# Optimization experiments

Measured on AMD Instinct MI355X. Metric: run time of the kernel, lower is better.

The kernel has to match this reference:

```python
import jax, jax.numpy as jnp
import numpy as np

B, S, HID = 2, 2048, 2560
NH, NKV, HD = 32, 8, 128
GROUPS = NH // NKV  # 4
THETA = 1000000.0
EPS = 1e-6


def setup_inputs() -> dict:
    key = jax.random.key(0)
    ks = jax.random.split(key, 6)
    inp = {
        "hidden_states": jax.random.normal(ks[0], (B, S, HID), jnp.float32),
        "Wq": jax.random.normal(ks[1], (HID, NH * HD), jnp.float32) * 0.02,
        "Wk": jax.random.normal(ks[2], (HID, NKV * HD), jnp.float32) * 0.02,
        "Wv": jax.random.normal(ks[3], (HID, NKV * HD), jnp.float32) * 0.02,
        "Wo": jax.random.normal(ks[4], (NH * HD, HID), jnp.float32) * 0.02,
        "q_norm_w": jnp.ones((HD,), jnp.float32),
        "k_norm_w": jnp.ones((HD,), jnp.float32),
        "position_ids": jnp.broadcast_to(jnp.arange(S, dtype=jnp.int64 if jax.config.jax_enable_x64 else jnp.int32), (B, S)),
    }
    return inp


def _rms_norm(x, w, eps=EPS):
    # per-head-dim RMSNorm in fp32, matching Qwen3RMSNorm
    xf = x.astype(jnp.float32)
    var = jnp.mean(xf * xf, axis=-1, keepdims=True)
    return (w * (xf * jax.lax.rsqrt(var + eps))).astype(x.dtype)


def _rotate_half(x):
    x1, x2 = jnp.split(x, 2, axis=-1)
    return jnp.concatenate((-x2, x1), axis=-1)


def _rope_tables(seq_len, pos_ids):
    inv_freq = 1.0 / (THETA ** (jnp.arange(0, HD, 2, dtype=jnp.float32) / HD))
    t = jnp.arange(seq_len, dtype=jnp.float32)
    freqs = jnp.einsum("i,j->ij", t, inv_freq)           # [S, HD/2]
    emb = jnp.concatenate((freqs, freqs), axis=-1)        # [S, HD]
    cos = jnp.cos(emb)[pos_ids][:, None, :, :]            # [B,1,S,HD]
    sin = jnp.sin(emb)[pos_ids][:, None, :, :]
    return cos, sin


def _attention(hidden_states, Wq, Wk, Wv, Wo, q_norm_w, k_norm_w, position_ids):
    b, s, _ = hidden_states.shape
    q = (hidden_states @ Wq).reshape(b, s, NH, HD).transpose(0, 2, 1, 3)   # [B,NH,S,HD]
    k = (hidden_states @ Wk).reshape(b, s, NKV, HD).transpose(0, 2, 1, 3)  # [B,NKV,S,HD]
    v = (hidden_states @ Wv).reshape(b, s, NKV, HD).transpose(0, 2, 1, 3)
    q = _rms_norm(q, q_norm_w)
    k = _rms_norm(k, k_norm_w)
    cos, sin = _rope_tables(s, position_ids)
    q = q * cos + _rotate_half(q) * sin
    k = k * cos + _rotate_half(k) * sin
    # GQA: group queries instead of repeating K/V (same math as repeat_kv)
    qg = q.reshape(b, NKV, GROUPS, s, HD)
    scale = 1.0 / np.sqrt(HD)
    scores = jnp.einsum("bhgqd,bhkd->bhgqk", qg, k) * scale  # [B,NKV,G,S,S]
    causal = jnp.tril(jnp.ones((s, s), bool))
    scores = jnp.where(causal, scores, jnp.finfo(scores.dtype).min)
    probs = jax.nn.softmax(scores.astype(jnp.float32), axis=-1).astype(q.dtype)
    out = jnp.einsum("bhgqk,bhkd->bhgqd", probs, v)          # [B,NKV,G,S,HD]
    out = out.reshape(b, NH, s, HD).transpose(0, 2, 1, 3).reshape(b, s, NH * HD)
    return out @ Wo                                          # [B,S,HID]


def reference(hidden_states, Wq, Wk, Wv, Wo, q_norm_w, k_norm_w, position_ids):
    return _attention(hidden_states, Wq, Wk, Wv, Wo, q_norm_w, k_norm_w, position_ids)
```

## Files before the change

### kernel.cpp

```cpp
#include <hip/hip_runtime.h>
#include <hip/hip_bf16.h>
#include <math.h>

#define B_ 2
#define S_ 2048
#define HID_ 2560
#define NH_ 32
#define NKV_ 8
#define HD_ 128

typedef __attribute__((ext_vector_type(8))) short bf16x8;
typedef __attribute__((ext_vector_type(4))) float f32x4;

union U8 { bf16x8 v; unsigned short u[8]; };

__device__ __forceinline__ unsigned short f2bf(float x) {
    unsigned u = __float_as_uint(x);
    u = u + 0x7FFF + ((u >> 16) & 1);
    return (unsigned short)(u >> 16);
}
__device__ __forceinline__ float bf2f(unsigned short h) {
    return __uint_as_float(((unsigned)h) << 16);
}

#define GL16(g, l)                                                             \
    __builtin_amdgcn_global_load_lds(                                          \
        (const __attribute__((address_space(1))) void*)(g),                    \
        (__attribute__((address_space(3))) void*)(l), 16, 0, 0)

__global__ void rope_table_kernel(float* __restrict__ cost, float* __restrict__ sint) {
    int t = blockIdx.x;
    int j = threadIdx.x;
    float invf = (float)pow(1.0e6, -(double)j / 64.0);
    float ang  = (float)t * invf;
    cost[t * 64 + j] = cosf(ang);
    sint[t * 64 + j] = sinf(ang);
}

__global__ __launch_bounds__(256) void convert_split(const float* __restrict__ in,
                                                     unsigned short* __restrict__ hi,
                                                     unsigned short* __restrict__ lo,
                                                     int n4) {
    int i = blockIdx.x * 256 + threadIdx.x;
    if (i >= n4) return;
    float4 v = *(const float4*)(in + (size_t)i * 4);
    ushort4 h, l;
    h.x = f2bf(v.x); l.x = f2bf(v.x - bf2f(h.x));
    h.y = f2bf(v.y); l.y = f2bf(v.y - bf2f(h.y));
    h.z = f2bf(v.z); l.z = f2bf(v.z - bf2f(h.z));
    h.w = f2bf(v.w); l.w = f2bf(v.w - bf2f(h.w));
    *(ushort4*)(hi + (size_t)i * 4) = h;
    *(ushort4*)(lo + (size_t)i * 4) = l;
}

__global__ __launch_bounds__(256) void convert_T(const float* __restrict__ in,
                                                 unsigned short* __restrict__ hiT,
                                                 unsigned short* __restrict__ loT,
                                                 int K, int N) {
    __shared__ float t[32][33];
    int k0 = blockIdx.y * 32, n0 = blockIdx.x * 32;
    int tr = threadIdx.x >> 5, tc = threadIdx.x & 31;
#pragma unroll
    for (int i = 0; i < 4; ++i)
        t[tr + i * 8][tc] = in[(size_t)(k0 + tr + i * 8) * N + n0 + tc];
    __syncthreads();
#pragma unroll
    for (int i = 0; i < 4; ++i) {
        int n = tr + i * 8, k = tc;
        float x = t[k][n];
        unsigned short h = f2bf(x);
        hiT[(size_t)(n0 + n) * K + k0 + k] = h;
        loT[(size_t)(n0 + n) * K + k0 + k] = f2bf(x - bf2f(h));
    }
}

__global__ __launch_bounds__(256) void gemm_split(const unsigned short* __restrict__ Ah,
                                                  const unsigned short* __restrict__ Al,
                                                  const unsigned short* __restrict__ Bh,
                                                  const unsigned short* __restrict__ Bl,
                                                  float* __restrict__ C,
                                                  int K, int N) {
    __shared__ unsigned short sAh[128 * 32], sAl[128 * 32];
    __shared__ unsigned short sBh[128 * 32], sBl[128 * 32];

    int tid  = threadIdx.x;
    int bn   = blockIdx.x, bm = blockIdx.y;
    int wave = tid >> 6, lane = tid & 63;
    int wr   = wave >> 1, wc = wave & 1;

    int r0  = tid >> 2;
    int cbp = (tid & 3) << 4;
    int e0  = (cbp ^ ((r0 & 3) << 4)) >> 1;

    const unsigned short* gAh = Ah + (size_t)(bm * 128 + r0) * K + e0;
    const unsigned short* gAl = Al + (size_t)(bm * 128 + r0) * K + e0;
    const unsigned short* gBh = Bh + (size_t)(bn * 128 + r0) * K + e0;
    const unsigned short* gBl = Bl + (size_t)(bn * 128 + r0) * K + e0;
    size_t rstep = (size_t)64 * K;

    char* lA_h = (char*)sAh + wave * 1024;
    char* lA_l = (char*)sAl + wave * 1024;
    char* lB_h = (char*)sBh + wave * 1024;
    char* lB_l = (char*)sBl + wave * 1024;

    int l15 = lane & 15, kh = lane >> 4;

    f32x4 acc[4][4];
#pragma unroll
    for (int i = 0; i < 4; ++i)
#pragma unroll
        for (int j = 0; j < 4; ++j) acc[i][j] = (f32x4)0.f;

    for (int k0 = 0; k0 < K; k0 += 32) {
        GL16(gAh + k0,         lA_h);
        GL16(gAh + rstep + k0, lA_h + 4096);
        GL16(gAl + k0,         lA_l);
        GL16(gAl + rstep + k0, lA_l + 4096);
        GL16(gBh + k0,         lB_h);
        GL16(gBh + rstep + k0, lB_h + 4096);
        GL16(gBl + k0,         lB_l);
        GL16(gBl + rstep + k0, lB_l + 4096);
        __syncthreads();

        bf16x8 fah[4], fal[4], fbh[4], fbl[4];
#pragma unroll
        for (int i = 0; i < 4; ++i) {
            int ar   = wr * 64 + i * 16 + l15;
            int arcb = (kh * 16) ^ ((ar & 3) << 4);
            fah[i] = *(const bf16x8*)((const char*)sAh + ar * 64 + arcb);
            fal[i] = *(const bf16x8*)((const char*)sAl + ar * 64 + arcb);
            int br   = wc * 64 + i * 16 + l15;
            int brcb = (kh * 16) ^ ((br & 3) << 4);
            fbh[i] = *(const bf16x8*)((const char*)sBh + br * 64 + brcb);
            fbl[i] = *(const bf16x8*)((const char*)sBl + br * 64 + brcb);
        }
#pragma unroll
        for (int mi = 0; mi < 4; ++mi)
#pragma unroll
            for (int ni = 0; ni < 4; ++ni) {
                acc[mi][ni] = __builtin_amdgcn_mfma_f32_16x16x32_bf16(fah[mi], fbh[ni], acc[mi][ni], 0, 0, 0);
                acc[mi][ni] = __builtin_amdgcn_mfma_f32_16x16x32_bf16(fah[mi], fbl[ni], acc[mi][ni], 0, 0, 0);
                acc[mi][ni] = __builtin_amdgcn_mfma_f32_16x16x32_bf16(fal[mi], fbh[ni], acc[mi][ni], 0, 0, 0);
            }
        __syncthreads();
    }

#pragma unroll
    for (int mi = 0; mi < 4; ++mi) {
        int row0 = bm * 128 + wr * 64 + mi * 16 + (lane >> 4) * 4;
#pragma unroll
        for (int ni = 0; ni < 4; ++ni) {
            int col = bn * 128 + wc * 64 + ni * 16 + (lane & 15);
#pragma unroll
            for (int j = 0; j < 4; ++j)
                C[(size_t)(row0 + j) * N + col] = acc[mi][ni][j];
        }
    }
}

__global__ __launch_bounds__(256) void rmsnorm_rope_kernel(
        const float* __restrict__ raw, const float* __restrict__ normw,
        const float* __restrict__ cost, const float* __restrict__ sint,
        const int* __restrict__ pos, float* __restrict__ outT,
        int H, int rowStride) {
    int wave = threadIdx.x >> 6;
    int lane = threadIdx.x & 63;
    int row  = blockIdx.x * 4 + wave;
    int h  = row % H;
    int bs = row / H;
    int b  = bs >> 11;
    int s  = bs & (S_ - 1);

    const float* x = raw + (size_t)bs * rowStride + h * HD_;
    float x1 = x[lane];
    float x2 = x[lane + 64];

    float ss = x1 * x1 + x2 * x2;
#pragma unroll
    for (int off = 32; off; off >>= 1) ss += __shfl_xor(ss, off);
    float inv = rsqrtf(ss * (1.0f / 128.0f) + 1e-6f);

    float n1 = x1 * inv * normw[lane];
    float n2 = x2 * inv * normw[lane + 64];

    int p  = pos[bs];
    float c  = cost[p * 64 + lane];
    float sn = sint[p * 64 + lane];
    float o1 = n1 * c - n2 * sn;
    float o2 = n2 * c + n1 * sn;

    float* o = outT + ((size_t)(b * H + h) * S_ + s) * HD_;
    o[lane]      = o1;
    o[lane + 64] = o2;
}

__global__ __launch_bounds__(256) void rmsnorm_rope_k_split(
        const float* __restrict__ raw, const float* __restrict__ normw,
        const float* __restrict__ cost, const float* __restrict__ sint,
        const int* __restrict__ pos,
        unsigned short* __restrict__ outH, unsigned short* __restrict__ outL) {
    int wave = threadIdx.x >> 6;
    int lane = threadIdx.x & 63;
    int row  = blockIdx.x * 4 + wave;
    int h  = row & 7;
    int bs = row >> 3;
    int b  = bs >> 11;
    int s  = bs & (S_ - 1);

    const float* x = raw + (size_t)bs * 2048 + h * HD_;
    float x1 = x[lane];
    float x2 = x[lane + 64];

    float ss = x1 * x1 + x2 * x2;
#pragma unroll
    for (int off = 32; off; off >>= 1) ss += __shfl_xor(ss, off);
    float inv = rsqrtf(ss * (1.0f / 128.0f) + 1e-6f);

    float n1 = x1 * inv * normw[lane];
    float n2 = x2 * inv * normw[lane + 64];

    int p  = pos[bs];
    float c  = cost[p * 64 + lane];
    float sn = sint[p * 64 + lane];
    float o1 = n1 * c - n2 * sn;
    float o2 = n2 * c + n1 * sn;

    size_t base = ((size_t)(b * NKV_ + h) * S_ + s) * HD_;
    unsigned short h1 = f2bf(o1), h2 = f2bf(o2);
    outH[base + lane]      = h1;
    outH[base + lane + 64] = h2;
    outL[base + lane]      = f2bf(o1 - bf2f(h1));
    outL[base + lane + 64] = f2bf(o2 - bf2f(h2));
}

__global__ __launch_bounds__(256) void vsplitT(const float* __restrict__ kv,
                                               unsigned short* __restrict__ vh,
                                               unsigned short* __restrict__ vl) {
    __shared__ float t[32][33];
    int s0 = blockIdx.x * 32;
    int d0 = blockIdx.y * 32;
    int bi = blockIdx.z;
    int b  = bi >> 3, kvh = bi & 7;
    int tr = threadIdx.x >> 5, tc = threadIdx.x & 31;
#pragma unroll
    for (int i = 0; i < 4; ++i)
        t[tr + i * 8][tc] = kv[(size_t)(b * S_ + s0 + tr + i * 8) * 2048 + 1024 + kvh * 128 + d0 + tc];
    __syncthreads();
#pragma unroll
    for (int i = 0; i < 4; ++i) {
        int d = tr + i * 8, s = tc;
        float x = t[s][d];
        size_t idx = ((size_t)(bi * 128 + d0 + d)) * S_ + s0 + s;
        unsigned short h = f2bf(x);
        vh[idx] = h;
        vl[idx] = f2bf(x - bf2f(h));
    }
}

__global__ __launch_bounds__(256) void attn_mfma(const float* __restrict__ qt,
                                                 const unsigned short* __restrict__ kth,
                                                 const unsigned short* __restrict__ ktl,
                                                 const unsigned short* __restrict__ vth,
                                                 const unsigned short* __restrict__ vtl,
                                                 float* __restrict__ aout) {
    __shared__ char lds[65536];
    char* Kh  = lds;
    char* Klo = lds + 16384;
    char* Vh  = lds + 32768;
    char* Vlo = lds + 49152;

    int tid = threadIdx.x, lane = tid & 63, w = tid >> 6;
    int g = lane >> 4, l15 = lane & 15;
    int qb = blockIdx.x, h = blockIdx.y, b = blockIdx.z;
    int kvh = h >> 2;
    int q0 = qb * 128;
    int wq = q0 + w * 32;
    int wrowmax = wq + 31;

    const float scale = 0.08838834764831845f;

    U8 qh[2][4], ql[2][4];
    {
        const float* qbase = qt + ((size_t)(b * NH_ + h) * S_ + wq) * HD_;
#pragma unroll
        for (int mt = 0; mt < 2; ++mt) {
            const float* qr = qbase + (mt * 16 + l15) * HD_;
#pragma unroll
            for (int ks = 0; ks < 4; ++ks) {
                float4 a0 = *(const float4*)(qr + ks * 32 + g * 8);
                float4 a1 = *(const float4*)(qr + ks * 32 + g * 8 + 4);
                float f[8] = {a0.x, a0.y, a0.z, a0.w, a1.x, a1.y, a1.z, a1.w};
#pragma unroll
                for (int e = 0; e < 8; ++e) {
                    float v = f[e] * scale;
                    unsigned short hi = f2bf(v);
                    qh[mt][ks].u[e] = hi;
                    ql[mt][ks].u[e] = f2bf(v - bf2f(hi));
                }
            }
        }
    }

    f32x4 O[2][8];
#pragma unroll
    for (int mt = 0; mt < 2; ++mt)
#pragma unroll
        for (int nt = 0; nt < 8; ++nt) O[mt][nt] = (f32x4)0.f;
    float m[2][4], l[2][4];
#pragma unroll
    for (int mt = 0; mt < 2; ++mt)
#pragma unroll
        for (int j = 0; j < 4; ++j) { m[mt][j] = -1e30f; l[mt][j] = 0.f; }

    int krow = (lane >> 4) + w * 4;
    int kcbp = (lane & 15) << 4;
    int vrow = (lane >> 3) + w * 8;
    int vcbp = (lane & 7) << 4;
    const unsigned short* kbh = kth + (size_t)(b * NKV_ + kvh) * S_ * HD_;
    const unsigned short* kbl = ktl + (size_t)(b * NKV_ + kvh) * S_ * HD_;
    const unsigned short* vbh = vth + (size_t)(b * NKV_ + kvh) * HD_ * S_;
    const unsigned short* vbl = vtl + (size_t)(b * NKV_ + kvh) * HD_ * S_;

    int kbmax = (q0 + 127) >> 6;
    for (int kb = 0; kb <= kbmax; ++kb) {
        __syncthreads();
#pragma unroll
        for (int is = 0; is < 4; ++is) {
            int kr = krow + is * 16;
            int ke = (kcbp ^ ((kr & 7) << 4)) >> 1;
            GL16(kbh + (size_t)(kb * 64 + kr) * HD_ + ke, Kh  + is * 4096 + w * 1024);
            GL16(kbl + (size_t)(kb * 64 + kr) * HD_ + ke, Klo + is * 4096 + w * 1024);
            int vr = vrow + is * 32;
            int ve = (vcbp ^ ((vr & 7) << 4)) >> 1;
            GL16(vbh + (size_t)vr * S_ + kb * 64 + ve, Vh  + is * 4096 + w * 1024);
            GL16(vbl + (size_t)vr * S_ + kb * 64 + ve, Vlo + is * 4096 + w * 1024);
        }
        __syncthreads();

        bool act = (kb * 64 <= wrowmax);
        f32x4 sc[2][4];
        if (act) {
#pragma unroll
            for (int mt = 0; mt < 2; ++mt)
#pragma unroll
                for (int nt = 0; nt < 4; ++nt) sc[mt][nt] = (f32x4)0.f;
#pragma unroll
            for (int ks = 0; ks < 4; ++ks) {
#pragma unroll
                for (int nt = 0; nt < 4; ++nt) {
                    int r  = nt * 16 + l15;
                    int cb = (ks * 64 + g * 16) ^ ((r & 7) << 4);
                    bf16x8 kf_h = *(const bf16x8*)(Kh  + r * 256 + cb);
                    bf16x8 kf_l = *(const bf16x8*)(Klo + r * 256 + cb);
#pragma unroll
                    for (int mt = 0; mt < 2; ++mt) {
                        sc[mt][nt] = __builtin_amdgcn_mfma_f32_16x16x32_bf16(qh[mt][ks].v, kf_h, sc[mt][nt], 0, 0, 0);
                        sc[mt][nt] = __builtin_amdgcn_mfma_f32_16x16x32_bf16(qh[mt][ks].v, kf_l, sc[mt][nt], 0, 0, 0);
                        sc[mt][nt] = __builtin_amdgcn_mfma_f32_16x16x32_bf16(ql[mt][ks].v, kf_h, sc[mt][nt], 0, 0, 0);
                    }
                }
            }
#pragma unroll
            for (int mt = 0; mt < 2; ++mt) {
#pragma unroll
                for (int j = 0; j < 4; ++j) {
                    int qrow = wq + mt * 16 + g * 4 + j;
#pragma unroll
                    for (int nt = 0; nt < 4; ++nt) {
                        int col = kb * 64 + nt * 16 + l15;
                        if (col > qrow) sc[mt][nt][j] = -1e30f;
                    }
                    float tmax = fmaxf(fmaxf(sc[mt][0][j], sc[mt][1][j]),
                                       fmaxf(sc[mt][2][j], sc[mt][3][j]));
#pragma unroll
                    for (int off = 8; off; off >>= 1) tmax = fmaxf(tmax, __shfl_xor(tmax, off));
                    float mn = fmaxf(m[mt][j], tmax);
                    float resc = __expf(m[mt][j] - mn);
                    m[mt][j] = mn;
                    float s0 = 0.f;
#pragma unroll
                    for (int nt = 0; nt < 4; ++nt) {
                        float p = __expf(sc[mt][nt][j] - mn);
                        sc[mt][nt][j] = p;
                        s0 += p;
                    }
#pragma unroll
                    for (int off = 8; off; off >>= 1) s0 += __shfl_xor(s0, off);
                    l[mt][j] = l[mt][j] * resc + s0;
#pragma unroll
                    for (int nt = 0; nt < 8; ++nt) O[mt][nt][j] *= resc;
                }
            }
        }
        __syncthreads();

        if (act) {
            char* P = lds + w * 8192;
#pragma unroll
            for (int mt = 0; mt < 2; ++mt)
#pragma unroll
                for (int nt = 0; nt < 4; ++nt)
#pragma unroll
                    for (int j = 0; j < 4; ++j) {
                        int prow = mt * 16 + g * 4 + j;
                        int pcol = nt * 16 + l15;
                        float pv = sc[mt][nt][j];
                        unsigned short ph = f2bf(pv);
                        unsigned short pl = f2bf(pv - bf2f(ph));
                        unsigned pk = (unsigned)ph | ((unsigned)pl << 16);
                        *(unsigned*)(P + prow * 256 + ((pcol * 4) ^ ((prow & 7) << 5))) = pk;
                    }
#pragma unroll
            for (int ks2 = 0; ks2 < 2; ++ks2) {
                U8 pah[2], pal[2];
#pragma unroll
                for (int mt = 0; mt < 2; ++mt) {
                    int arow = mt * 16 + l15;
                    int ab   = arow * 256 + ((ks2 * 128 + g * 32) ^ ((arow & 7) << 5));
                    uint4 p0 = *(const uint4*)(P + ab);
                    uint4 p1 = *(const uint4*)(P + ab + 16);
                    unsigned pw[8] = {p0.x, p0.y, p0.z, p0.w, p1.x, p1.y, p1.z, p1.w};
#pragma unroll
                    for (int e = 0; e < 8; ++e) {
                        pah[mt].u[e] = (unsigned short)(pw[e] & 0xFFFF);
                        pal[mt].u[e] = (unsigned short)(pw[e] >> 16);
                    }
                }
#pragma unroll
                for (int nt = 0; nt < 8; ++nt) {
                    int r  = nt * 16 + l15;
                    int cb = (ks2 * 64 + g * 16) ^ ((r & 7) << 4);
                    bf16x8 vf_h = *(const bf16x8*)(Vh  + r * 128 + cb);
                    bf16x8 vf_l = *(const bf16x8*)(Vlo + r * 128 + cb);
#pragma unroll
                    for (int mt = 0; mt < 2; ++mt) {
                        O[mt][nt] = __builtin_amdgcn_mfma_f32_16x16x32_bf16(pah[mt].v, vf_h, O[mt][nt], 0, 0, 0);
                        O[mt][nt] = __builtin_amdgcn_mfma_f32_16x16x32_bf16(pal[mt].v, vf_h, O[mt][nt], 0, 0, 0);
                        O[mt][nt] = __builtin_amdgcn_mfma_f32_16x16x32_bf16(pah[mt].v, vf_l, O[mt][nt], 0, 0, 0);
                    }
                }
            }
        }
    }

#pragma unroll
    for (int mt = 0; mt < 2; ++mt) {
        float invl[4];
#pragma unroll
        for (int j = 0; j < 4; ++j) invl[j] = 1.f / l[mt][j];
#pragma unroll
        for (int nt = 0; nt < 8; ++nt)
#pragma unroll
            for (int j = 0; j < 4; ++j) {
                int sq  = wq + mt * 16 + g * 4 + j;
                int col = h * 128 + nt * 16 + l15;
                aout[(size_t)(b * S_ + sq) * 4096 + col] = O[mt][nt][j] * invl[j];
            }
    }
}

extern "C" void kernel_launch(void* const* d_in, const int* in_sizes, int n_in,
                              void* d_out, int out_size, void* d_ws, size_t ws_size,
                              hipStream_t stream) {
    const float* X   = (const float*)d_in[0];
    const float* Wq  = (const float*)d_in[1];
    const float* Wk  = (const float*)d_in[2];
    const float* Wv  = (const float*)d_in[3];
    const float* Wo  = (const float*)d_in[4];
    const float* qnw = (const float*)d_in[5];
    const float* knw = (const float*)d_in[6];
    const int*   pos = (const int*)d_in[7];
    float* out = (float*)d_out;

    char* ws = (char*)d_ws;
    float*          cost = (float*)(ws + 0);
    float*          sint = (float*)(ws + 524288);
    unsigned short* Xh   = (unsigned short*)(ws + 1048576);
    unsigned short* Xl   = (unsigned short*)(ws + 22020096);
    unsigned short* WqH  = (unsigned short*)(ws + 42991616);
    unsigned short* WqL  = (unsigned short*)(ws + 63963136);
    unsigned short* KVH  = (unsigned short*)(ws + 84934656);
    unsigned short* KVL  = (unsigned short*)(ws + 95420416);
    unsigned short* WoH  = (unsigned short*)(ws + 105906176);
    unsigned short* WoL  = (unsigned short*)(ws + 126877696);
    float*          qraw = (float*)(ws + 147849216);
    float*          kv   = (float*)(ws + 214958080);
    float*          qt   = (float*)(ws + 1048576);
    unsigned short* vtTh = (unsigned short*)(ws + 68157440);
    unsigned short* vtTl = (unsigned short*)(ws + 76546048);
    unsigned short* kth  = (unsigned short*)(ws + 84934656);
    unsigned short* ktl  = (unsigned short*)(ws + 93323264);
    unsigned short* Ah2  = (unsigned short*)(ws + 1048576);
    unsigned short* Al2  = (unsigned short*)(ws + 34603008);

    rope_table_kernel<<<S_, 64, 0, stream>>>(cost, sint);

    convert_split<<<(4096 * 2560 / 4 + 255) / 256, 256, 0, stream>>>(X, Xh, Xl, 4096 * 2560 / 4);
    convert_T<<<dim3(4096 / 32, 2560 / 32), 256, 0, stream>>>(Wq, WqH, WqL, HID_, 4096);
    convert_T<<<dim3(1024 / 32, 2560 / 32), 256, 0, stream>>>(Wk, KVH, KVL, HID_, 1024);
    convert_T<<<dim3(1024 / 32, 2560 / 32), 256, 0, stream>>>(Wv, KVH + 1024 * 2560, KVL + 1024 * 2560, HID_, 1024);
    convert_T<<<dim3(2560 / 32, 4096 / 32), 256, 0, stream>>>(Wo, WoH, WoL, 4096, 2560);

    gemm_split<<<dim3(4096 / 128, 4096 / 128), 256, 0, stream>>>(Xh, Xl, WqH, WqL, qraw, HID_, 4096);
    gemm_split<<<dim3(2048 / 128, 4096 / 128), 256, 0, stream>>>(Xh, Xl, KVH, KVL, kv, HID_, 2048);

    rmsnorm_rope_kernel<<<(B_ * S_ * NH_) / 4, 256, 0, stream>>>(qraw, qnw, cost, sint, pos, qt, NH_, 4096);
    rmsnorm_rope_k_split<<<(B_ * S_ * NKV_) / 4, 256, 0, stream>>>(kv, knw, cost, sint, pos, kth, ktl);
    vsplitT<<<dim3(64, 4, 16), 256, 0, stream>>>(kv, vtTh, vtTl);

    attn_mfma<<<dim3(16, 32, 2), 256, 0, stream>>>(qt, kth, ktl, vtTh, vtTl, qraw);

    convert_split<<<(4096 * 4096 / 4 + 255) / 256, 256, 0, stream>>>(qraw, Ah2, Al2, 4096 * 4096 / 4);
    gemm_split<<<dim3(2560 / 128, 4096 / 128), 256, 0, stream>>>(Ah2, Al2, WoH, WoL, out, 4096, 2560);
}
```

Baseline: 1.741 ms.

## Read K/V directly from global, drop V-lo term, fuse output bf16 split

The attention kernel stops staging K/V tiles in shared memory with block-wide barriers. Each wave now reads K and V fragments directly from global memory and runs only as many key blocks as its own rows need, with query blocks launched in reverse order so the heaviest ones start first. The P·V_lo MFMA term and the V-lo input are dropped, which cuts matrix work but lowers precision of the split-bf16 emulation. The attention output is written directly as hi/lo bf16, removing the separate convert_split pass before the output projection.

Measured after the change: 2.122 ms. 21.8% more time.

```diff
diff --git a/kernel.cpp b/kernel.cpp
--- a/kernel.cpp
+++ b/kernel.cpp
@@ -261,21 +261,15 @@
                                                  const unsigned short* __restrict__ kth,
                                                  const unsigned short* __restrict__ ktl,
                                                  const unsigned short* __restrict__ vth,
-                                                 const unsigned short* __restrict__ vtl,
-                                                 float* __restrict__ aout) {
-    __shared__ char lds[65536];
-    char* Kh  = lds;
-    char* Klo = lds + 16384;
-    char* Vh  = lds + 32768;
-    char* Vlo = lds + 49152;
+                                                 unsigned short* __restrict__ outH,
+                                                 unsigned short* __restrict__ outL) {
+    __shared__ char Plds[32768];
 
     int tid = threadIdx.x, lane = tid & 63, w = tid >> 6;
     int g = lane >> 4, l15 = lane & 15;
-    int qb = blockIdx.x, h = blockIdx.y, b = blockIdx.z;
+    int qb = 15 - blockIdx.x, h = blockIdx.y, b = blockIdx.z;
     int kvh = h >> 2;
-    int q0 = qb * 128;
-    int wq = q0 + w * 32;
-    int wrowmax = wq + 31;
+    int wq = qb * 128 + w * 32;
 
     const float scale = 0.08838834764831845f;
 
@@ -312,132 +306,102 @@
 #pragma unroll
         for (int j = 0; j < 4; ++j) { m[mt][j] = -1e30f; l[mt][j] = 0.f; }
 
-    int krow = (lane >> 4) + w * 4;
-    int kcbp = (lane & 15) << 4;
-    int vrow = (lane >> 3) + w * 8;
-    int vcbp = (lane & 7) << 4;
     const unsigned short* kbh = kth + (size_t)(b * NKV_ + kvh) * S_ * HD_;
     const unsigned short* kbl = ktl + (size_t)(b * NKV_ + kvh) * S_ * HD_;
     const unsigned short* vbh = vth + (size_t)(b * NKV_ + kvh) * HD_ * S_;
-    const unsigned short* vbl = vtl + (size_t)(b * NKV_ + kvh) * HD_ * S_;
-
-    int kbmax = (q0 + 127) >> 6;
+    char* P = Plds + w * 8192;
+
+    int kbmax = (wq + 31) >> 6;
     for (int kb = 0; kb <= kbmax; ++kb) {
-        __syncthreads();
-#pragma unroll
-        for (int is = 0; is < 4; ++is) {
-            int kr = krow + is * 16;
-            int ke = (kcbp ^ ((kr & 7) << 4)) >> 1;
-            GL16(kbh + (size_t)(kb * 64 + kr) * HD_ + ke, Kh  + is * 4096 + w * 1024);
-            GL16(kbl + (size_t)(kb * 64 + kr) * HD_ + ke, Klo + is * 4096 + w * 1024);
-            int vr = vrow + is * 32;
-            int ve = (vcbp ^ ((vr & 7) << 4)) >> 1;
-            GL16(vbh + (size_t)vr * S_ + kb * 64 + ve, Vh  + is * 4096 + w * 1024);
-            GL16(vbl + (size_t)vr * S_ + kb * 64 + ve, Vlo + is * 4096 + w * 1024);
-        }
-        __syncthreads();
-
-        bool act = (kb * 64 <= wrowmax);
         f32x4 sc[2][4];
-        if (act) {
-#pragma unroll
-            for (int mt = 0; mt < 2; ++mt)
-#pragma unroll
-                for (int nt = 0; nt < 4; ++nt) sc[mt][nt] = (f32x4)0.f;
-#pragma unroll
-            for (int ks = 0; ks < 4; ++ks) {
+#pragma unroll
+        for (int mt = 0; mt < 2; ++mt)
+#pragma unroll
+            for (int nt = 0; nt < 4; ++nt) sc[mt][nt] = (f32x4)0.f;
+#pragma unroll
+        for (int ks = 0; ks < 4; ++ks) {
+#pragma unroll
+            for (int nt = 0; nt < 4; ++nt) {
+                size_t koff = (size_t)(kb * 64 + nt * 16 + l15) * HD_ + ks * 32 + g * 8;
+                bf16x8 kf_h = *(const bf16x8*)(kbh + koff);
+                bf16x8 kf_l = *(const bf16x8*)(kbl + koff);
+#pragma unroll
+                for (int mt = 0; mt < 2; ++mt) {
+                    sc[mt][nt] = __builtin_amdgcn_mfma_f32_16x16x32_bf16(qh[mt][ks].v, kf_h, sc[mt][nt], 0, 0, 0);
+                    sc[mt][nt] = __builtin_amdgcn_mfma_f32_16x16x32_bf16(qh[mt][ks].v, kf_l, sc[mt][nt], 0, 0, 0);
+                    sc[mt][nt] = __builtin_amdgcn_mfma_f32_16x16x32_bf16(ql[mt][ks].v, kf_h, sc[mt][nt], 0, 0, 0);
+                }
+            }
+        }
+#pragma unroll
+        for (int mt = 0; mt < 2; ++mt) {
+#pragma unroll
+            for (int j = 0; j < 4; ++j) {
+                int qrow = wq + mt * 16 + g * 4 + j;
 #pragma unroll
                 for (int nt = 0; nt < 4; ++nt) {
-                    int r  = nt * 16 + l15;
-                    int cb = (ks * 64 + g * 16) ^ ((r & 7) << 4);
-                    bf16x8 kf_h = *(const bf16x8*)(Kh  + r * 256 + cb);
-                    bf16x8 kf_l = *(const bf16x8*)(Klo + r * 256 + cb);
-#pragma unroll
-                    for (int mt = 0; mt < 2; ++mt) {
-                        sc[mt][nt] = __builtin_amdgcn_mfma_f32_16x16x32_bf16(qh[mt][ks].v, kf_h, sc[mt][nt], 0, 0, 0);
-                        sc[mt][nt] = __builtin_amdgcn_mfma_f32_16x16x32_bf16(qh[mt][ks].v, kf_l, sc[mt][nt], 0, 0, 0);
-                        sc[mt][nt] = __builtin_amdgcn_mfma_f32_16x16x32_bf16(ql[mt][ks].v, kf_h, sc[mt][nt], 0, 0, 0);
-                    }
-                }
-            }
+                    int col = kb * 64 + nt * 16 + l15;
+                    if (col > qrow) sc[mt][nt][j] = -1e30f;
+                }
+                float tmax = fmaxf(fmaxf(sc[mt][0][j], sc[mt][1][j]),
+                                   fmaxf(sc[mt][2][j], sc[mt][3][j]));
+#pragma unroll
+                for (int off = 8; off; off >>= 1) tmax = fmaxf(tmax, __shfl_xor(tmax, off));
+                float mn = fmaxf(m[mt][j], tmax);
+                float resc = __expf(m[mt][j] - mn);
+                m[mt][j] = mn;
+                float s0 = 0.f;
+#pragma unroll
+                for (int nt = 0; nt < 4; ++nt) {
+                    float p = __expf(sc[mt][nt][j] - mn);
+                    sc[mt][nt][j] = p;
+                    s0 += p;
+                }
+#pragma unroll
+                for (int off = 8; off; off >>= 1) s0 += __shfl_xor(s0, off);
+                l[mt][j] = l[mt][j] * resc + s0;
+#pragma unroll
+                for (int nt = 0; nt < 8; ++nt) O[mt][nt][j] *= resc;
+            }
+        }
+#pragma unroll
+        for (int mt = 0; mt < 2; ++mt)
+#pragma unroll
+            for (int nt = 0; nt < 4; ++nt)
+#pragma unroll
+                for (int j = 0; j < 4; ++j) {
+                    int prow = mt * 16 + g * 4 + j;
+                    int pcol = nt * 16 + l15;
+                    float pv = sc[mt][nt][j];
+                    unsigned short ph = f2bf(pv);
+                    unsigned short pl = f2bf(pv - bf2f(ph));
+                    unsigned pk = (unsigned)ph | ((unsigned)pl << 16);
+                    *(unsigned*)(P + prow * 256 + ((pcol * 4) ^ ((prow & 7) << 5))) = pk;
+                }
+#pragma unroll
+        for (int ks2 = 0; ks2 < 2; ++ks2) {
+            U8 pah[2], pal[2];
 #pragma unroll
             for (int mt = 0; mt < 2; ++mt) {
-#pragma unroll
-                for (int j = 0; j < 4; ++j) {
-                    int qrow = wq + mt * 16 + g * 4 + j;
-#pragma unroll
-                    for (int nt = 0; nt < 4; ++nt) {
-                        int col = kb * 64 + nt * 16 + l15;
-                        if (col > qrow) sc[mt][nt][j] = -1e30f;
-                    }
-                    float tmax = fmaxf(fmaxf(sc[mt][0][j], sc[mt][1][j]),
-                                       fmaxf(sc[mt][2][j], sc[mt][3][j]));
-#pragma unroll
-                    for (int off = 8; off; off >>= 1) tmax = fmaxf(tmax, __shfl_xor(tmax, off));
-                    float mn = fmaxf(m[mt][j], tmax);
-                    float resc = __expf(m[mt][j] - mn);
-                    m[mt][j] = mn;
-                    float s0 = 0.f;
-#pragma unroll
-                    for (int nt = 0; nt < 4; ++nt) {
-                        float p = __expf(sc[mt][nt][j] - mn);
-                        sc[mt][nt][j] = p;
-                        s0 += p;
-                    }
-#pragma unroll
-                    for (int off = 8; off; off >>= 1) s0 += __shfl_xor(s0, off);
-                    l[mt][j] = l[mt][j] * resc + s0;
-#pragma unroll
-                    for (int nt = 0; nt < 8; ++nt) O[mt][nt][j] *= resc;
-                }
-            }
-        }
-        __syncthreads();
-
-        if (act) {
-            char* P = lds + w * 8192;
-#pragma unroll
-            for (int mt = 0; mt < 2; ++mt)
-#pragma unroll
-                for (int nt = 0; nt < 4; ++nt)
-#pragma unroll
-                    for (int j = 0; j < 4; ++j) {
-                        int prow = mt * 16 + g * 4 + j;
-                        int pcol = nt * 16 + l15;
-                        float pv = sc[mt][nt][j];
-                        unsigned short ph = f2bf(pv);
-                        unsigned short pl = f2bf(pv - bf2f(ph));
-                        unsigned pk = (unsigned)ph | ((unsigned)pl << 16);
-                        *(unsigned*)(P + prow * 256 + ((pcol * 4) ^ ((prow & 7) << 5))) = pk;
-                    }
-#pragma unroll
-            for (int ks2 = 0; ks2 < 2; ++ks2) {
-                U8 pah[2], pal[2];
+                int arow = mt * 16 + l15;
+                int ab   = arow * 256 + ((ks2 * 128 + g * 32) ^ ((arow & 7) << 5));
+                uint4 p0 = *(const uint4*)(P + ab);
+                uint4 p1 = *(const uint4*)(P + ab + 16);
+                unsigned pw[8] = {p0.x, p0.y, p0.z, p0.w, p1.x, p1.y, p1.z, p1.w};
+#pragma unroll
+                for (int e = 0; e < 8; ++e) {
+                    pah[mt].u[e] = (unsigned short)(pw[e] & 0xFFFF);
+                    pal[mt].u[e] = (unsigned short)(pw[e] >> 16);
+                }
+            }
+#pragma unroll
+            for (int nt = 0; nt < 8; ++nt) {
+                size_t voff = (size_t)(nt * 16 + l15) * S_ + kb * 64 + ks2 * 32 + g * 8;
+                bf16x8 vf_h = *(const bf16x8*)(vbh + voff);
 #pragma unroll
                 for (int mt = 0; mt < 2; ++mt) {
-                    int arow = mt * 16 + l15;
-                    int ab   = arow * 256 + ((ks2 * 128 + g * 32) ^ ((arow & 7) << 5));
-                    uint4 p0 = *(const uint4*)(P + ab);
-                    uint4 p1 = *(const uint4*)(P + ab + 16);
-                    unsigned pw[8] = {p0.x, p0.y, p0.z, p0.w, p1.x, p1.y, p1.z, p1.w};
-#pragma unroll
-                    for (int e = 0; e < 8; ++e) {
-                        pah[mt].u[e] = (unsigned short)(pw[e] & 0xFFFF);
-                        pal[mt].u[e] = (unsigned short)(pw[e] >> 16);
-                    }
-                }
-#pragma unroll
-                for (int nt = 0; nt < 8; ++nt) {
-                    int r  = nt * 16 + l15;
-                    int cb = (ks2 * 64 + g * 16) ^ ((r & 7) << 4);
-                    bf16x8 vf_h = *(const bf16x8*)(Vh  + r * 128 + cb);
-                    bf16x8 vf_l = *(const bf16x8*)(Vlo + r * 128 + cb);
-#pragma unroll
-                    for (int mt = 0; mt < 2; ++mt) {
-                        O[mt][nt] = __builtin_amdgcn_mfma_f32_16x16x32_bf16(pah[mt].v, vf_h, O[mt][nt], 0, 0, 0);
-                        O[mt][nt] = __builtin_amdgcn_mfma_f32_16x16x32_bf16(pal[mt].v, vf_h, O[mt][nt], 0, 0, 0);
-                        O[mt][nt] = __builtin_amdgcn_mfma_f32_16x16x32_bf16(pah[mt].v, vf_l, O[mt][nt], 0, 0, 0);
-                    }
+                    O[mt][nt] = __builtin_amdgcn_mfma_f32_16x16x32_bf16(pah[mt].v, vf_h, O[mt][nt], 0, 0, 0);
+                    O[mt][nt] = __builtin_amdgcn_mfma_f32_16x16x32_bf16(pal[mt].v, vf_h, O[mt][nt], 0, 0, 0);
                 }
             }
         }
@@ -454,7 +418,11 @@
             for (int j = 0; j < 4; ++j) {
                 int sq  = wq + mt * 16 + g * 4 + j;
                 int col = h * 128 + nt * 16 + l15;
-                aout[(size_t)(b * S_ + sq) * 4096 + col] = O[mt][nt][j] * invl[j];
+                size_t idx = (size_t)(b * S_ + sq) * 4096 + col;
+                float v = O[mt][nt][j] * invl[j];
+                unsigned short hh = f2bf(v);
+                outH[idx] = hh;
+                outL[idx] = f2bf(v - bf2f(hh));
             }
     }
 }
@@ -490,8 +458,8 @@
     unsigned short* vtTl = (unsigned short*)(ws + 76546048);
     unsigned short* kth  = (unsigned short*)(ws + 84934656);
     unsigned short* ktl  = (unsigned short*)(ws + 93323264);
-    unsigned short* Ah2  = (unsigned short*)(ws + 1048576);
-    unsigned short* Al2  = (unsigned short*)(ws + 34603008);
+    unsigned short* Ah2  = (unsigned short*)(ws + 147849216);
+    unsigned short* Al2  = (unsigned short*)(ws + 181403648);
 
     rope_table_kernel<<<S_, 64, 0, stream>>>(cost, sint);
 
@@ -508,8 +476,7 @@
     rmsnorm_rope_k_split<<<(B_ * S_ * NKV_) / 4, 256, 0, stream>>>(kv, knw, cost, sint, pos, kth, ktl);
     vsplitT<<<dim3(64, 4, 16), 256, 0, stream>>>(kv, vtTh, vtTl);
 
-    attn_mfma<<<dim3(16, 32, 2), 256, 0, stream>>>(qt, kth, ktl, vtTh, vtTl, qraw);
-
-    convert_split<<<(4096 * 4096 / 4 + 255) / 256, 256, 0, stream>>>(qraw, Ah2, Al2, 4096 * 4096 / 4);
+    attn_mfma<<<dim3(16, 32, 2), 256, 0, stream>>>(qt, kth, ktl, vtTh, Ah2, Al2);
+
     gemm_split<<<dim3(2560 / 128, 4096 / 128), 256, 0, stream>>>(Ah2, Al2, WoH, WoL, out, 4096, 2560);
 }
```
